# Kernel optimization log

Hardware: AMD Instinct MI355X
Metric: run time of the kernel (lower is better)

## Reference

```python
import jax, jax.numpy as jnp
import numpy as np

N, S, D = 8, 1024, 512      # batch, seq_len, in_dim
H, KD, VD, OD = 8, 64, 64, 512  # heads, key_dim, value_dim, out_dim
GRAPH_WEIGHT = 0.5
NEG_INF = float('-inf')


def setup_inputs() -> dict:
    key = jax.random.key(0)
    ks = jax.random.split(key, 9)
    return {
        "x":    jax.random.normal(ks[0], (N, S, D), jnp.float32),
        "Wk":   jax.random.normal(ks[1], (H, D, KD), jnp.float32) * 0.02,
        "bk":   jax.random.normal(ks[2], (H, KD), jnp.float32) * 0.02,
        "Wv":   jax.random.normal(ks[3], (H, D, VD), jnp.float32) * 0.02,
        "bv":   jax.random.normal(ks[4], (H, VD), jnp.float32) * 0.02,
        "Wout": jax.random.normal(ks[5], (H * VD, OD), jnp.float32) * 0.02,
        "bout": jax.random.normal(ks[6], (OD,), jnp.float32) * 0.02,
        "graph": jax.random.normal(ks[7], (S, S), jnp.float32),
        "knn": 64,
    }


def reference(x, Wk, bk, Wv, bv, Wout, bout, graph, knn):
    # Per-head key/value projections (heads vectorized on leading axis h).
    k = jnp.einsum('nsd,hdk->hnsk', x, Wk) + bk[:, None, None, :]   # (H,N,S,KD)
    v = jnp.einsum('nsd,hdv->hnsv', x, Wv) + bv[:, None, None, :]   # (H,N,S,VD)
    q = k  # self-attention: query = key

    # att_unnorm = (q . k) / sqrt(key_dim)  -> (H,N,S,S)
    att = jnp.einsum('hnqk,hntk->hnqt', q, k) / np.sqrt(KD).astype(np.float32)

    # Causal mask (equivalent to the Python loop att[:, i, i+1:] = -inf).
    causal = jnp.tril(jnp.ones((S, S), dtype=bool))
    att = jnp.where(causal, att, NEG_INF)

    # knn top-k pooling: keep top-knn entries along the last axis, rest -> -inf.
    topv = jax.lax.top_k(att, knn)[0]                  # (H,N,S,knn)
    kth = topv[..., -1:]                               # kth largest per row
    att = jnp.where(att >= kth, att, NEG_INF)

    p = jax.nn.softmax(att, axis=-1)

    # Graph-weighted attention blend (graph is row-softmaxed at init time).
    att_graph = jax.nn.softmax(graph, axis=-1)         # (S,S)
    p = GRAPH_WEIGHT * att_graph + (1.0 - GRAPH_WEIGHT) * p

    # y_h = att @ value, then concat heads and output projection.
    y = jnp.einsum('hnqt,hntv->hnqv', p, v)            # (H,N,S,VD)
    y = y.transpose(1, 2, 0, 3).reshape(N, S, H * VD)  # head-major concat
    return y @ Wout + bout
```

## Files before the change

### kernel.cpp

```cpp
#include <hip/hip_runtime.h>
#include <math.h>

#define NB 8
#define SL 1024
#define DI 512
#define HH 8
#define KDN 64
#define VDN 64
#define ODN 512
#define ATT_SCALE 0.125f

#define KLO_OFF 2097152u
#define V_OFF   4194304u
#define G_OFF   8388608u
#define Y_OFF   9437184u

#define ORD_NEG_INF 0x007FFFFFu

typedef __attribute__((ext_vector_type(8))) short bf16x8;
typedef __attribute__((ext_vector_type(4))) float f32x4;

__device__ __forceinline__ unsigned fordu(float f) {
  unsigned b = __float_as_uint(f);
  return b ^ ((b & 0x80000000u) ? 0xFFFFFFFFu : 0x80000000u);
}
__device__ __forceinline__ float ifordu(unsigned k) {
  unsigned b = k ^ ((k & 0x80000000u) ? 0x80000000u : 0xFFFFFFFFu);
  return __uint_as_float(b);
}
__device__ __forceinline__ unsigned short f2bf(float f) {
  unsigned u = __float_as_uint(f);
  unsigned r = (u + 0x7FFFu + ((u >> 16) & 1u)) >> 16;
  return (unsigned short)r;
}

__global__ __launch_bounds__(256) void kvproj_kernel(
    const float* __restrict__ x, const float* __restrict__ Wk, const float* __restrict__ bk,
    const float* __restrict__ Wv, const float* __restrict__ bv, float* __restrict__ ws)
{
  __shared__ float xs[64][68];
  __shared__ float wks[64][68];
  __shared__ float wvs[64][68];
  const int tid = threadIdx.x;
  const int tx = tid & 15, ty = tid >> 4;
  const int m0 = blockIdx.x * 64;
  const int h = blockIdx.y;
  const float* wkb = Wk + (size_t)h * (DI * KDN);
  const float* wvb = Wv + (size_t)h * (DI * VDN);
  float ak[4][4] = {{0.f}};
  float av[4][4] = {{0.f}};
  for (int dt = 0; dt < DI / 64; ++dt) {
    __syncthreads();
#pragma unroll
    for (int it = 0; it < 4; ++it) {
      const int r = ty + it * 16;
      const int c = tx * 4;
      *(float4*)&xs[r][c]  = *(const float4*)&x[(size_t)(m0 + r) * DI + dt * 64 + c];
      *(float4*)&wks[r][c] = *(const float4*)&wkb[(size_t)(dt * 64 + r) * KDN + c];
      *(float4*)&wvs[r][c] = *(const float4*)&wvb[(size_t)(dt * 64 + r) * VDN + c];
    }
    __syncthreads();
#pragma unroll 4
    for (int dd = 0; dd < 64; ++dd) {
      float a[4];
#pragma unroll
      for (int i = 0; i < 4; ++i) a[i] = xs[ty * 4 + i][dd];
      const float4 bkv = *(const float4*)&wks[dd][tx * 4];
      const float4 bvv = *(const float4*)&wvs[dd][tx * 4];
      const float bkj[4] = {bkv.x, bkv.y, bkv.z, bkv.w};
      const float bvj[4] = {bvv.x, bvv.y, bvv.z, bvv.w};
#pragma unroll
      for (int i = 0; i < 4; ++i) {
#pragma unroll
        for (int j = 0; j < 4; ++j) {
          ak[i][j] = __fmaf_rn(a[i], bkj[j], ak[i][j]);
          av[i][j] = __fmaf_rn(a[i], bvj[j], av[i][j]);
        }
      }
    }
  }
  const int n = m0 >> 10;
  const int s0 = m0 & 1023;
  float* vb = ws + V_OFF;
  unsigned short* khi = (unsigned short*)ws;
  unsigned short* klo = (unsigned short*)(ws + KLO_OFF);
#pragma unroll
  for (int i = 0; i < 4; ++i) {
    const int s = s0 + ty * 4 + i;
    float4 vv;
    vv.x = av[i][0] + bv[h * VDN + tx * 4 + 0];
    vv.y = av[i][1] + bv[h * VDN + tx * 4 + 1];
    vv.z = av[i][2] + bv[h * VDN + tx * 4 + 2];
    vv.w = av[i][3] + bv[h * VDN + tx * 4 + 3];
    *(float4*)&vb[((size_t)(h * NB + n) * SL + s) * VDN + tx * 4] = vv;
    union { unsigned short u[4]; uint2 v2; } ph, pl;
#pragma unroll
    for (int j = 0; j < 4; ++j) {
      const float kf = ak[i][j] + bk[h * KDN + tx * 4 + j];
      const unsigned short h16 = f2bf(kf);
      const float hf = __uint_as_float(((unsigned)h16) << 16);
      ph.u[j] = h16;
      pl.u[j] = f2bf(kf - hf);
    }
    const size_t koff = ((size_t)(h * NB + n) * SL + s) * KDN + tx * 4;
    *(uint2*)&khi[koff] = ph.v2;
    *(uint2*)&klo[koff] = pl.v2;
  }
}

__global__ __launch_bounds__(256) void gsoftmax_kernel(const float* __restrict__ gin, float* __restrict__ ws)
{
  float* gout = ws + G_OFF;
  const int row = blockIdx.x;
  const int tid = threadIdx.x;
  const int lane = tid & 63, wave = tid >> 6;
  __shared__ float red[4];
  __shared__ float red2[4];
  float v[4];
  float m = -INFINITY;
#pragma unroll
  for (int i = 0; i < 4; ++i) {
    v[i] = gin[(size_t)row * SL + tid + i * 256];
    m = fmaxf(m, v[i]);
  }
#pragma unroll
  for (int off = 32; off; off >>= 1) m = fmaxf(m, __shfl_xor(m, off));
  if (lane == 0) red[wave] = m;
  __syncthreads();
  m = fmaxf(fmaxf(red[0], red[1]), fmaxf(red[2], red[3]));
  float e[4];
  float s = 0.f;
#pragma unroll
  for (int i = 0; i < 4; ++i) { e[i] = __expf(v[i] - m); s += e[i]; }
#pragma unroll
  for (int off = 32; off; off >>= 1) s += __shfl_xor(s, off);
  if (lane == 0) red2[wave] = s;
  __syncthreads();
  s = red2[0] + red2[1] + red2[2] + red2[3];
  const float inv = 1.0f / s;
#pragma unroll
  for (int i = 0; i < 4; ++i) gout[(size_t)row * SL + tid + i * 256] = e[i] * inv;
}

__global__ __launch_bounds__(256, 8) void attn_kernel(float* __restrict__ ws, const int* __restrict__ knn_p)
{
  __shared__ float S[16][260];
  const int tid = threadIdx.x;
  const int lane = tid & 63;
  const int wave = tid >> 6;
  const int q0 = blockIdx.x * 16;
  const int hn = blockIdx.y;
  const int h = hn >> 3, n = hn & 7;
  const int K = knn_p[0];
  const unsigned short* khi = (const unsigned short*)ws + (size_t)hn * SL * KDN;
  const unsigned short* klo = (const unsigned short*)(ws + KLO_OFF) + (size_t)hn * SL * KDN;
  const float* vb = ws + V_OFF + (size_t)hn * (SL * VDN);
  float* y = ws + Y_OFF;

  const int col = lane & 15, grp = lane >> 4;
  const bf16x8 a0h = *(const bf16x8*)&khi[(size_t)(q0 + col) * KDN + grp * 8];
  const bf16x8 a1h = *(const bf16x8*)&khi[(size_t)(q0 + col) * KDN + 32 + grp * 8];
  const bf16x8 a0l = *(const bf16x8*)&klo[(size_t)(q0 + col) * KDN + grp * 8];
  const bf16x8 a1l = *(const bf16x8*)&klo[(size_t)(q0 + col) * KDN + 32 + grp * 8];

  const int T = q0 / 16 + 1;
  const int rbase = wave * 4;

  float ev[4][8][2];
#pragma unroll
  for (int rr = 0; rr < 4; ++rr)
#pragma unroll
    for (int c = 0; c < 8; ++c) {
      ev[rr][c][0] = __uint_as_float(ORD_NEG_INF);
      ev[rr][c][1] = __uint_as_float(ORD_NEG_INF);
    }

#pragma unroll
  for (int ph = 0; ph < 4; ++ph) {
    const int tlo = ph * 16;
    const int thi = (T < tlo + 16) ? T : (tlo + 16);
    if (thi > tlo) {
      __syncthreads();
      for (int ti = tlo + wave; ti < thi; ti += 4) {
        const int t0 = ti * 16;
        const size_t bo = (size_t)(t0 + col) * KDN + grp * 8;
        const bf16x8 b0h = *(const bf16x8*)&khi[bo];
        const bf16x8 b1h = *(const bf16x8*)&khi[bo + 32];
        const bf16x8 b0l = *(const bf16x8*)&klo[bo];
        const bf16x8 b1l = *(const bf16x8*)&klo[bo + 32];
        f32x4 d = {0.f, 0.f, 0.f, 0.f};
        d = __builtin_amdgcn_mfma_f32_16x16x32_bf16(a0h, b0h, d, 0, 0, 0);
        d = __builtin_amdgcn_mfma_f32_16x16x32_bf16(a1h, b1h, d, 0, 0, 0);
        d = __builtin_amdgcn_mfma_f32_16x16x32_bf16(a0h, b0l, d, 0, 0, 0);
        d = __builtin_amdgcn_mfma_f32_16x16x32_bf16(a1h, b1l, d, 0, 0, 0);
        d = __builtin_amdgcn_mfma_f32_16x16x32_bf16(a0l, b0h, d, 0, 0, 0);
        d = __builtin_amdgcn_mfma_f32_16x16x32_bf16(a1l, b1h, d, 0, 0, 0);
        d = __builtin_amdgcn_mfma_f32_16x16x32_bf16(a0l, b0l, d, 0, 0, 0);
        d = __builtin_amdgcn_mfma_f32_16x16x32_bf16(a1l, b1l, d, 0, 0, 0);
        const int tl = t0 - ph * 256 + col;
#pragma unroll
        for (int r = 0; r < 4; ++r) S[grp * 4 + r][tl] = d[r];
      }
      __syncthreads();
#pragma unroll
      for (int rr = 0; rr < 4; ++rr) {
        const int q = q0 + rbase + rr;
        const int cmr = q >> 7;
#pragma unroll
        for (int cc = 0; cc < 2; ++cc) {
          const int c = ph * 2 + cc;
          if (c <= cmr) {
            const float2 sv = *(const float2*)&S[rbase + rr][cc * 128 + lane * 2];
            const int t0 = c * 128 + lane * 2;
            const unsigned k0 = (t0     <= q) ? fordu(sv.x * ATT_SCALE) : ORD_NEG_INF;
            const unsigned k1 = (t0 + 1 <= q) ? fordu(sv.y * ATT_SCALE) : ORD_NEG_INF;
            ev[rr][c][0] = __uint_as_float(k0);
            ev[rr][c][1] = __uint_as_float(k1);
          }
        }
      }
    }
  }
  __syncthreads();

  float* elist = (float*)((char*)&S[0][0] + wave * 768);
  unsigned short* tlist = (unsigned short*)(elist + 128);

#pragma unroll
  for (int rr = 0; rr < 4; ++rr) {
    const int q = q0 + rbase + rr;

    unsigned u[16];
#pragma unroll
    for (int c = 0; c < 8; ++c) {
      u[c * 2]     = __float_as_uint(ev[rr][c][0]);
      u[c * 2 + 1] = __float_as_uint(ev[rr][c][1]);
    }

    unsigned lmax = u[0];
#pragma unroll
    for (int i = 1; i < 16; ++i) lmax = lmax > u[i] ? lmax : u[i];
    unsigned mk = lmax, t0k = lmax;
#pragma unroll
    for (int off = 32; off; off >>= 1) {
      const unsigned om = (unsigned)__shfl_xor((int)mk, off);
      const unsigned ot = (unsigned)__shfl_xor((int)t0k, off);
      mk = mk > om ? mk : om;
      t0k = t0k < ot ? t0k : ot;
    }
    const float m = ifordu(mk);

    unsigned kth;
    if (q < K) {
      kth = ORD_NEG_INF;
    } else {
      unsigned lo = (K <= 64) ? t0k : 0u;
      unsigned hi = mk;
      while (lo < hi) {
        const unsigned mid = lo + ((hi - lo + 1) >> 1);
        int cnt = 0;
#pragma unroll
        for (int i = 0; i < 16; ++i)
          cnt += (int)__popcll(__ballot(u[i] >= mid));
        if (cnt >= K) lo = mid; else hi = mid - 1;
      }
      kth = lo;
    }

    float Z = 0.f;
#pragma unroll
    for (int c = 0; c < 8; ++c) {
#pragma unroll
      for (int j = 0; j < 2; ++j) {
        const unsigned k = u[c * 2 + j];
        float e = 0.f;
        if (k >= kth) e = __expf(ifordu(k) - m);
        ev[rr][c][j] = e;
        Z += e;
      }
    }
#pragma unroll
    for (int off = 32; off; off >>= 1) Z += __shfl_xor(Z, off);

    const unsigned long long lt = (1ull << lane) - 1ull;
    int cnt = 0;
#pragma unroll
    for (int c = 0; c < 8; ++c) {
#pragma unroll
      for (int j = 0; j < 2; ++j) {
        const float e = ev[rr][c][j];
        const unsigned long long msk = __ballot(e > 0.f);
        if (e > 0.f) {
          const int pos = cnt + (int)__popcll(msk & lt);
          if (pos < 128) {
            elist[pos] = e;
            tlist[pos] = (unsigned short)(c * 128 + lane * 2 + j);
          }
        }
        cnt += (int)__popcll(msk);
      }
    }
    cnt = (cnt < 128) ? cnt : 128;

    float yacc = 0.f;
    int i2 = 0;
    for (; i2 + 4 <= cnt; i2 += 4) {
      const float4 e4 = *(const float4*)&elist[i2];
      const ushort4 t4 = *(const ushort4*)&tlist[i2];
      yacc = __fmaf_rn(e4.x, vb[(size_t)t4.x * VDN + lane], yacc);
      yacc = __fmaf_rn(e4.y, vb[(size_t)t4.y * VDN + lane], yacc);
      yacc = __fmaf_rn(e4.z, vb[(size_t)t4.z * VDN + lane], yacc);
      yacc = __fmaf_rn(e4.w, vb[(size_t)t4.w * VDN + lane], yacc);
    }
    for (; i2 < cnt; ++i2) {
      yacc = __fmaf_rn(elist[i2], vb[(size_t)tlist[i2] * VDN + lane], yacc);
    }
    y[((size_t)(n * SL + q)) * ODN + h * VDN + lane] = yacc * (0.5f / Z);
  }
}

__global__ __launch_bounds__(256) void gv_kernel(float* __restrict__ ws)
{
  __shared__ float as_[64][68];
  __shared__ float bs_[64][68];
  const int tid = threadIdx.x;
  const int tx = tid & 15, ty = tid >> 4;
  const int q0 = blockIdx.x * 64;
  const int hn = blockIdx.y;
  const int h = hn >> 3, n = hn & 7;
  const float* g = ws + G_OFF;
  const float* vb = ws + V_OFF + (size_t)hn * (SL * VDN);
  float* y = ws + Y_OFF;
  float acc[4][4] = {{0.f}};
  for (int kt = 0; kt < 16; ++kt) {
    __syncthreads();
#pragma unroll
    for (int it = 0; it < 4; ++it) {
      const int r = ty + it * 16;
      const int c = tx * 4;
      *(float4*)&as_[r][c] = *(const float4*)&g[(size_t)(q0 + r) * SL + kt * 64 + c];
      *(float4*)&bs_[r][c] = *(const float4*)&vb[(size_t)(kt * 64 + r) * VDN + c];
    }
    __syncthreads();
#pragma unroll 4
    for (int dd = 0; dd < 64; ++dd) {
      float a[4];
#pragma unroll
      for (int i = 0; i < 4; ++i) a[i] = as_[ty * 4 + i][dd];
      const float4 b4 = *(const float4*)&bs_[dd][tx * 4];
      const float bj[4] = {b4.x, b4.y, b4.z, b4.w};
#pragma unroll
      for (int i = 0; i < 4; ++i)
#pragma unroll
        for (int j = 0; j < 4; ++j)
          acc[i][j] = __fmaf_rn(a[i], bj[j], acc[i][j]);
    }
  }
#pragma unroll
  for (int i = 0; i < 4; ++i) {
    const size_t off = ((size_t)(n * SL + q0 + ty * 4 + i)) * ODN + h * VDN + tx * 4;
    float4 cur = *(float4*)&y[off];
    cur.x += 0.5f * acc[i][0];
    cur.y += 0.5f * acc[i][1];
    cur.z += 0.5f * acc[i][2];
    cur.w += 0.5f * acc[i][3];
    *(float4*)&y[off] = cur;
  }
}

__global__ __launch_bounds__(256) void out_kernel(
    const float* __restrict__ Wout, const float* __restrict__ bout,
    const float* __restrict__ ws, float* __restrict__ out)
{
  __shared__ float as_[64][68];
  __shared__ float bs_[64][68];
  const int tid = threadIdx.x;
  const int tx = tid & 15, ty = tid >> 4;
  const int od0 = blockIdx.x * 64;
  const int m0 = blockIdx.y * 64;
  const float* y = ws + Y_OFF;
  float acc[4][4] = {{0.f}};
  for (int kt = 0; kt < 8; ++kt) {
    __syncthreads();
#pragma unroll
    for (int it = 0; it < 4; ++it) {
      const int r = ty + it * 16;
      const int c = tx * 4;
      *(float4*)&as_[r][c] = *(const float4*)&y[(size_t)(m0 + r) * ODN + kt * 64 + c];
      *(float4*)&bs_[r][c] = *(const float4*)&Wout[(size_t)(kt * 64 + r) * ODN + od0 + c];
    }
    __syncthreads();
#pragma unroll 4
    for (int dd = 0; dd < 64; ++dd) {
      float a[4];
#pragma unroll
      for (int i = 0; i < 4; ++i) a[i] = as_[ty * 4 + i][dd];
      const float4 b4 = *(const float4*)&bs_[dd][tx * 4];
      const float bj[4] = {b4.x, b4.y, b4.z, b4.w};
#pragma unroll
      for (int i = 0; i < 4; ++i)
#pragma unroll
        for (int j = 0; j < 4; ++j)
          acc[i][j] = __fmaf_rn(a[i], bj[j], acc[i][j]);
    }
  }
#pragma unroll
  for (int i = 0; i < 4; ++i) {
    float4 o4;
    o4.x = acc[i][0] + bout[od0 + tx * 4 + 0];
    o4.y = acc[i][1] + bout[od0 + tx * 4 + 1];
    o4.z = acc[i][2] + bout[od0 + tx * 4 + 2];
    o4.w = acc[i][3] + bout[od0 + tx * 4 + 3];
    *(float4*)&out[(size_t)(m0 + ty * 4 + i) * ODN + od0 + tx * 4] = o4;
  }
}

extern "C" void kernel_launch(void* const* d_in, const int* in_sizes, int n_in,
                              void* d_out, int out_size, void* d_ws, size_t ws_size,
                              hipStream_t stream)
{
  const float* x     = (const float*)d_in[0];
  const float* Wk    = (const float*)d_in[1];
  const float* bk    = (const float*)d_in[2];
  const float* Wv    = (const float*)d_in[3];
  const float* bv    = (const float*)d_in[4];
  const float* Wout  = (const float*)d_in[5];
  const float* bout  = (const float*)d_in[6];
  const float* graph = (const float*)d_in[7];
  const int*   knn   = (const int*)d_in[8];
  float* out = (float*)d_out;
  float* ws  = (float*)d_ws;

  kvproj_kernel<<<dim3(128, 8), 256, 0, stream>>>(x, Wk, bk, Wv, bv, ws);
  gsoftmax_kernel<<<dim3(1024), 256, 0, stream>>>(graph, ws);
  attn_kernel<<<dim3(64, 64), 256, 0, stream>>>(ws, knn);
  gv_kernel<<<dim3(16, 64), 256, 0, stream>>>(ws);
  out_kernel<<<dim3(8, 128), 256, 0, stream>>>(Wout, bout, ws, out);
}
```

Measured before the change: 570.0 us.

## Run output projection on bf16x3 MFMA with pre-transposed split Wout

Replaces the scalar FP32 shared-memory GEMM in the output projection with MFMA 16x16x32 bf16 instructions. Each activation and weight is split into hi+lo bf16 parts, and three products are taken to approximate FP32 accuracy. A new prep kernel transposes Wout and splits it into those parts, writing them into the start of the workspace, a region the attention kernel's K data occupied earlier. The attention kernel's launch bounds also change from 8 to 4 waves per SIMD, which relaxes register pressure at the cost of occupancy.

```diff
diff --git a/kernel.cpp b/kernel.cpp
--- a/kernel.cpp
+++ b/kernel.cpp
@@ -32,6 +32,9 @@
   unsigned u = __float_as_uint(f);
   unsigned r = (u + 0x7FFFu + ((u >> 16) & 1u)) >> 16;
   return (unsigned short)r;
+}
+__device__ __forceinline__ float bf2f(unsigned short h) {
+  return __uint_as_float(((unsigned)h) << 16);
 }
 
 __global__ __launch_bounds__(256) void kvproj_kernel(
@@ -98,9 +101,8 @@
     for (int j = 0; j < 4; ++j) {
       const float kf = ak[i][j] + bk[h * KDN + tx * 4 + j];
       const unsigned short h16 = f2bf(kf);
-      const float hf = __uint_as_float(((unsigned)h16) << 16);
       ph.u[j] = h16;
-      pl.u[j] = f2bf(kf - hf);
+      pl.u[j] = f2bf(kf - bf2f(h16));
     }
     const size_t koff = ((size_t)(h * NB + n) * SL + s) * KDN + tx * 4;
     *(uint2*)&khi[koff] = ph.v2;
@@ -142,7 +144,7 @@
   for (int i = 0; i < 4; ++i) gout[(size_t)row * SL + tid + i * 256] = e[i] * inv;
 }
 
-__global__ __launch_bounds__(256, 8) void attn_kernel(float* __restrict__ ws, const int* __restrict__ knn_p)
+__global__ __launch_bounds__(256, 4) void attn_kernel(float* __restrict__ ws, const int* __restrict__ knn_p)
 {
   __shared__ float S[16][260];
   const int tid = threadIdx.x;
@@ -368,50 +370,83 @@
   }
 }
 
+__global__ __launch_bounds__(256) void wtprep_kernel(const float* __restrict__ Wout, float* __restrict__ ws)
+{
+  __shared__ float tile[64][65];
+  unsigned short* wth = (unsigned short*)ws;
+  unsigned short* wtl = wth + ODN * ODN;
+  const int t = threadIdx.x;
+  const int od0 = blockIdx.x * 64;
+  const int k0 = blockIdx.y * 64;
+  const int r = t >> 2, c4 = (t & 3) * 16;
+#pragma unroll
+  for (int j = 0; j < 4; ++j) {
+    *(float4*)&tile[r][c4 + j * 4] = *(const float4*)&Wout[(size_t)(k0 + r) * ODN + od0 + c4 + j * 4];
+  }
+  __syncthreads();
+  union { unsigned short u[16]; uint4 v[2]; } hi, lo;
+#pragma unroll
+  for (int j = 0; j < 16; ++j) {
+    const float f = tile[c4 + j][r];
+    const unsigned short h16 = f2bf(f);
+    hi.u[j] = h16;
+    lo.u[j] = f2bf(f - bf2f(h16));
+  }
+  const size_t o = (size_t)(od0 + r) * ODN + k0 + c4;
+  *(uint4*)&wth[o] = hi.v[0];
+  *(uint4*)&wth[o + 8] = hi.v[1];
+  *(uint4*)&wtl[o] = lo.v[0];
+  *(uint4*)&wtl[o + 8] = lo.v[1];
+}
+
 __global__ __launch_bounds__(256) void out_kernel(
-    const float* __restrict__ Wout, const float* __restrict__ bout,
-    const float* __restrict__ ws, float* __restrict__ out)
-{
-  __shared__ float as_[64][68];
-  __shared__ float bs_[64][68];
+    const float* __restrict__ bout, const float* __restrict__ ws, float* __restrict__ out)
+{
+  const unsigned short* wth = (const unsigned short*)ws;
+  const unsigned short* wtl = wth + ODN * ODN;
+  const float* y = ws + Y_OFF;
   const int tid = threadIdx.x;
-  const int tx = tid & 15, ty = tid >> 4;
+  const int lane = tid & 63;
+  const int wave = tid >> 6;
+  const int col = lane & 15, grp = lane >> 4;
   const int od0 = blockIdx.x * 64;
-  const int m0 = blockIdx.y * 64;
-  const float* y = ws + Y_OFF;
-  float acc[4][4] = {{0.f}};
-  for (int kt = 0; kt < 8; ++kt) {
-    __syncthreads();
-#pragma unroll
-    for (int it = 0; it < 4; ++it) {
-      const int r = ty + it * 16;
-      const int c = tx * 4;
-      *(float4*)&as_[r][c] = *(const float4*)&y[(size_t)(m0 + r) * ODN + kt * 64 + c];
-      *(float4*)&bs_[r][c] = *(const float4*)&Wout[(size_t)(kt * 64 + r) * ODN + od0 + c];
-    }
-    __syncthreads();
-#pragma unroll 4
-    for (int dd = 0; dd < 64; ++dd) {
-      float a[4];
-#pragma unroll
-      for (int i = 0; i < 4; ++i) a[i] = as_[ty * 4 + i][dd];
-      const float4 b4 = *(const float4*)&bs_[dd][tx * 4];
-      const float bj[4] = {b4.x, b4.y, b4.z, b4.w};
-#pragma unroll
-      for (int i = 0; i < 4; ++i)
-#pragma unroll
-        for (int j = 0; j < 4; ++j)
-          acc[i][j] = __fmaf_rn(a[i], bj[j], acc[i][j]);
-    }
-  }
-#pragma unroll
-  for (int i = 0; i < 4; ++i) {
-    float4 o4;
-    o4.x = acc[i][0] + bout[od0 + tx * 4 + 0];
-    o4.y = acc[i][1] + bout[od0 + tx * 4 + 1];
-    o4.z = acc[i][2] + bout[od0 + tx * 4 + 2];
-    o4.w = acc[i][3] + bout[od0 + tx * 4 + 3];
-    *(float4*)&out[(size_t)(m0 + ty * 4 + i) * ODN + od0 + tx * 4] = o4;
+  const int m0 = blockIdx.y * 64 + wave * 16;
+
+  f32x4 acc[4];
+#pragma unroll
+  for (int odt = 0; odt < 4; ++odt) acc[odt] = (f32x4){0.f, 0.f, 0.f, 0.f};
+
+  const float* yrow = y + (size_t)(m0 + col) * ODN + grp * 8;
+  for (int ks = 0; ks < 16; ++ks) {
+    const float4 ya = *(const float4*)&yrow[ks * 32];
+    const float4 yb = *(const float4*)&yrow[ks * 32 + 4];
+    union { unsigned short u[8]; bf16x8 v; } ah, al;
+    const float yf[8] = {ya.x, ya.y, ya.z, ya.w, yb.x, yb.y, yb.z, yb.w};
+#pragma unroll
+    for (int j = 0; j < 8; ++j) {
+      const unsigned short h16 = f2bf(yf[j]);
+      ah.u[j] = h16;
+      al.u[j] = f2bf(yf[j] - bf2f(h16));
+    }
+#pragma unroll
+    for (int odt = 0; odt < 4; ++odt) {
+      const size_t bo = (size_t)(od0 + odt * 16 + col) * ODN + ks * 32 + grp * 8;
+      const bf16x8 bh = *(const bf16x8*)&wth[bo];
+      const bf16x8 bl = *(const bf16x8*)&wtl[bo];
+      acc[odt] = __builtin_amdgcn_mfma_f32_16x16x32_bf16(ah.v, bh, acc[odt], 0, 0, 0);
+      acc[odt] = __builtin_amdgcn_mfma_f32_16x16x32_bf16(ah.v, bl, acc[odt], 0, 0, 0);
+      acc[odt] = __builtin_amdgcn_mfma_f32_16x16x32_bf16(al.v, bh, acc[odt], 0, 0, 0);
+    }
+  }
+
+#pragma unroll
+  for (int odt = 0; odt < 4; ++odt) {
+    const int od = od0 + odt * 16 + col;
+    const float bo = bout[od];
+#pragma unroll
+    for (int r = 0; r < 4; ++r) {
+      out[(size_t)(m0 + grp * 4 + r) * ODN + od] = acc[odt][r] + bo;
+    }
   }
 }
 
@@ -434,6 +469,7 @@
   kvproj_kernel<<<dim3(128, 8), 256, 0, stream>>>(x, Wk, bk, Wv, bv, ws);
   gsoftmax_kernel<<<dim3(1024), 256, 0, stream>>>(graph, ws);
   attn_kernel<<<dim3(64, 64), 256, 0, stream>>>(ws, knn);
+  wtprep_kernel<<<dim3(8, 8), 256, 0, stream>>>(Wout, ws);
   gv_kernel<<<dim3(16, 64), 256, 0, stream>>>(ws);
-  out_kernel<<<dim3(8, 128), 256, 0, stream>>>(Wout, bout, ws, out);
-}
+  out_kernel<<<dim3(8, 128), 256, 0, stream>>>(bout, ws, out);
+}
```

After: 604.0 us. 1.06x slower.
